# Performance work log

Measured on AMD Instinct MI355X. Metric: run time of the kernel, lower is better.

## Reference

```python
import jax, jax.numpy as jnp
import numpy as np

TEMPERATURE = 0.07
NEG_INF = -1e9


def setup_inputs() -> dict:
    key = jax.random.key(0)
    k1, k2, k3, k4, k5 = jax.random.split(key, 5)
    B, L, H = 64, 256, 64
    query_embs = jax.random.normal(k1, (B, L, H), dtype=jnp.float32)
    key_embs = jax.random.normal(k2, (B, L, H), dtype=jnp.float32)
    labels = jax.random.randint(k3, (B,), 0, 2, dtype=jnp.int64)
    q_mask = jax.random.randint(k4, (B, L), 0, 2, dtype=jnp.int32)
    k_mask = jax.random.randint(k5, (B, L), 0, 2, dtype=jnp.int32)
    return {"query_embs": query_embs, "key_embs": key_embs, "labels": labels,
            "q_mask": q_mask, "k_mask": k_mask}


def reference(query_embs, key_embs, labels, q_mask, k_mask):
    # ColBERT-style late interaction over all B x B pairs.
    # sim: (B_q, B_k, Lq, Lk) token-level dot products.
    sim = jnp.einsum('bqh,ckh->bcqk', query_embs, key_embs)
    # Mask out padded key tokens before the max over key positions.
    sim = jnp.where(k_mask[None, :, None, :].astype(bool), sim, NEG_INF)
    maxsim = jnp.max(sim, axis=-1)                      # (B_q, B_k, Lq)
    qm = q_mask[:, None, :].astype(maxsim.dtype)        # (B_q, 1, Lq)
    scores = jnp.sum(maxsim * qm, axis=-1) / TEMPERATURE  # (B_q, B_k)
    # Cross-entropy on rows with labels==1, target = diagonal index.
    logp = jax.nn.log_softmax(scores, axis=-1)
    B = scores.shape[0]
    diag = logp[jnp.arange(B), jnp.arange(B)]           # (B,)
    w = labels.astype(scores.dtype)
    denom = jnp.maximum(jnp.sum(w), 1.0)
    return -jnp.sum(w * diag) / denom
```

## Files before the change

kernel.cpp:

```cpp
#include <hip/hip_runtime.h>
#include <math.h>

#define PB 64
#define PL 256
#define PH 64
#define TEMP 0.07f
#define NEG_INF_F (-1e9f)

#define KSTRIDE 72
#define KROWB   (KSTRIDE * 2)
#define KSLAB   (PL * KSTRIDE)
#define BGRP    2

typedef short short8 __attribute__((ext_vector_type(8)));
typedef float f32x4 __attribute__((ext_vector_type(4)));

__device__ __forceinline__ unsigned short f32_to_bf16(float f) {
    unsigned int u = __float_as_uint(f);
    u += 0x7FFFu + ((u >> 16) & 1u);
    return (unsigned short)(u >> 16);
}

__global__ __launch_bounds__(256)
void prep_kernel(const float* __restrict__ Q,
                 const float* __restrict__ K,
                 const int*   __restrict__ kmask,
                 const int*   __restrict__ qmask,
                 unsigned short* __restrict__ Qcomp,
                 unsigned short* __restrict__ Kcomp,
                 int* __restrict__ nvK,
                 int* __restrict__ nvQ) {
    const int tid  = threadIdx.x;
    const int lane = tid & 63;
    const int wave = tid >> 6;
    __shared__ int posArr[PL];
    __shared__ int wcnt[4];

    const bool isQ = (blockIdx.x >= 256);
    const int  bid = isQ ? (blockIdx.x - 256) : blockIdx.x;
    const int  idx     = bid >> 2;
    const int  quarter = bid & 3;

    const int* mask = isQ ? (qmask + idx * PL) : (kmask + idx * PL);
    const int km = mask[tid];
    unsigned long long bal = __ballot(km != 0);
    int within = __popcll(bal & ((1ull << lane) - 1ull));
    if (lane == 0) wcnt[wave] = __popcll(bal);
    __syncthreads();
    int base = 0;
    #pragma unroll
    for (int w = 0; w < 4; ++w) base += (w < wave) ? wcnt[w] : 0;
    posArr[tid] = km ? (base + within) : -1;
    const int nv = wcnt[0] + wcnt[1] + wcnt[2] + wcnt[3];
    __syncthreads();

    const int sub = lane >> 4;
    const int cl  = lane & 15;
    const float* src = (isQ ? Q : K) + (size_t)idx * PL * PH;

    if (!isQ) {
        unsigned short* slab = Kcomp + (size_t)idx * KSLAB;
        #pragma unroll
        for (int it = 0; it < 4; ++it) {
            int r = quarter * 64 + it * 16 + wave * 4 + sub;
            int p = posArr[r];
            if (p >= 0) {
                float4 v = *(const float4*)(src + (size_t)r * PH + cl * 4);
                ushort4 o;
                o.x = f32_to_bf16(v.x); o.y = f32_to_bf16(v.y);
                o.z = f32_to_bf16(v.z); o.w = f32_to_bf16(v.w);
                *(ushort4*)(slab + (size_t)p * KSTRIDE + cl * 4) = o;
            }
        }
        const int rows16 = (nv + 15) & ~15;
        const int padChunks = (rows16 - nv) * 16;
        if (tid < padChunks) {
            int row = nv + (tid >> 4);
            if (row >= quarter * 64 && row < quarter * 64 + 64)
                *(ushort4*)(slab + (size_t)row * KSTRIDE + (tid & 15) * 4) = (ushort4){0, 0, 0, 0};
        }
        if (quarter == 0 && tid == 0) nvK[idx] = nv;
    } else {
        unsigned short* slab = Qcomp + (size_t)idx * PL * PH;
        #pragma unroll
        for (int it = 0; it < 4; ++it) {
            int r = quarter * 64 + it * 16 + wave * 4 + sub;
            int p = posArr[r];
            if (p >= 0) {
                float4 v = *(const float4*)(src + (size_t)r * PH + cl * 4);
                ushort4 o;
                o.x = f32_to_bf16(v.x); o.y = f32_to_bf16(v.y);
                o.z = f32_to_bf16(v.z); o.w = f32_to_bf16(v.w);
                *(ushort4*)(slab + (size_t)p * PH + cl * 4) = o;
            }
        }
        #pragma unroll
        for (int it = 0; it < 4; ++it) {
            int id2 = it * 256 + tid;
            int row = quarter * 64 + (id2 >> 4);
            if (row >= nv)
                *(ushort4*)(slab + (size_t)row * PH + (id2 & 15) * 4) = (ushort4){0, 0, 0, 0};
        }
        if (quarter == 0 && tid == 0) nvQ[idx] = nv;
    }
}

__global__ __launch_bounds__(256)
void colbert_scores_mfma(const unsigned short* __restrict__ Qcomp,
                         const unsigned short* __restrict__ Kcomp,
                         const int*   __restrict__ nvK,
                         const int*   __restrict__ nvQ,
                         float*       __restrict__ scores) {
    const int c  = blockIdx.x;
    const int bg = blockIdx.y;
    const int tid  = threadIdx.x;
    const int wave = tid >> 6;
    const int lane = tid & 63;
    const int n    = lane & 15;
    const int g    = (lane >> 4) & 3;

    __shared__ __align__(16) unsigned short Ks[PL * KSTRIDE];
    __shared__ float red[BGRP][4];

    const int nv     = nvK[c];
    const int rows16 = (nv + 15) & ~15;
    const int nbytes = rows16 * KROWB;

    {
        const char* gsrc  = (const char*)(Kcomp + (size_t)c * KSLAB);
        char*       lbase = (char*)Ks;
        const int nchunks = (nbytes + 4095) >> 12;
        for (int it = 0; it < nchunks; ++it) {
            int off = it * 4096 + tid * 16;
            __builtin_amdgcn_global_load_lds(
                (const __attribute__((address_space(1))) unsigned int*)(gsrc + off),
                (__attribute__((address_space(3)))       unsigned int*)(lbase + off),
                16, 0, 0);
        }
    }

    const int b0 = bg * BGRP;
    const int nq0 = nvQ[b0];
    const int nq1 = nvQ[b0 + 1];
    const int ntQP = ((max(nq0, nq1)) + 31) >> 5;

    __syncthreads();

    const f32x4 ZERO4 = (f32x4){0.f, 0.f, 0.f, 0.f};
    const int ntFull   = nv >> 4;
    const int tailCols = nv & 15;
    const unsigned short* krow0 = &Ks[n * KSTRIDE + g * 8];
    const float biasv = (n < tailCols) ? 0.0f : NEG_INF_F;
    const f32x4 BIAS4 = (f32x4){biasv, biasv, biasv, biasv};

    float partial[BGRP] = {0.0f, 0.0f};

    for (int qp = wave; qp < ntQP; qp += 4) {
        short8 aA[BGRP][2][2];
        #pragma unroll
        for (int bi = 0; bi < BGRP; ++bi) {
            const unsigned short* Qrow = Qcomp + ((size_t)(b0 + bi) * PL + qp * 32 + n) * PH + g * 8;
            aA[bi][0][0] = *(const short8*)(Qrow);
            aA[bi][0][1] = *(const short8*)(Qrow + 32);
            aA[bi][1][0] = *(const short8*)(Qrow + 16 * PH);
            aA[bi][1][1] = *(const short8*)(Qrow + 16 * PH + 32);
        }

        float maxv[BGRP][2][4];
        #pragma unroll
        for (int bi = 0; bi < BGRP; ++bi)
            #pragma unroll
            for (int t = 0; t < 2; ++t)
                #pragma unroll
                for (int r = 0; r < 4; ++r) maxv[bi][t][r] = NEG_INF_F;

        int ct = 0;
        for (; ct + 1 < ntFull; ct += 2) {
            const unsigned short* ka = krow0 + ct * 16 * KSTRIDE;
            short8 kA0 = *(const short8*)(ka);
            short8 kA1 = *(const short8*)(ka + 32);
            short8 kB0 = *(const short8*)(ka + 16 * KSTRIDE);
            short8 kB1 = *(const short8*)(ka + 16 * KSTRIDE + 32);

            #pragma unroll
            for (int bi = 0; bi < BGRP; ++bi)
                #pragma unroll
                for (int t = 0; t < 2; ++t) {
                    f32x4 accA = __builtin_amdgcn_mfma_f32_16x16x32_bf16(aA[bi][t][0], kA0, ZERO4, 0, 0, 0);
                    accA = __builtin_amdgcn_mfma_f32_16x16x32_bf16(aA[bi][t][1], kA1, accA, 0, 0, 0);
                    f32x4 accB = __builtin_amdgcn_mfma_f32_16x16x32_bf16(aA[bi][t][0], kB0, ZERO4, 0, 0, 0);
                    accB = __builtin_amdgcn_mfma_f32_16x16x32_bf16(aA[bi][t][1], kB1, accB, 0, 0, 0);
                    #pragma unroll
                    for (int r = 0; r < 4; ++r)
                        maxv[bi][t][r] = fmaxf(maxv[bi][t][r], fmaxf(accA[r], accB[r]));
                }
        }

        if (ntFull & 1) {
            const unsigned short* ka = krow0 + ct * 16 * KSTRIDE;
            short8 k0 = *(const short8*)(ka);
            short8 k1 = *(const short8*)(ka + 32);
            #pragma unroll
            for (int bi = 0; bi < BGRP; ++bi)
                #pragma unroll
                for (int t = 0; t < 2; ++t) {
                    f32x4 acc = __builtin_amdgcn_mfma_f32_16x16x32_bf16(aA[bi][t][0], k0, ZERO4, 0, 0, 0);
                    acc = __builtin_amdgcn_mfma_f32_16x16x32_bf16(aA[bi][t][1], k1, acc, 0, 0, 0);
                    #pragma unroll
                    for (int r = 0; r < 4; ++r)
                        maxv[bi][t][r] = fmaxf(maxv[bi][t][r], acc[r]);
                }
            ct++;
        }

        if (tailCols) {
            const unsigned short* ka = krow0 + ct * 16 * KSTRIDE;
            short8 k0 = *(const short8*)(ka);
            short8 k1 = *(const short8*)(ka + 32);
            #pragma unroll
            for (int bi = 0; bi < BGRP; ++bi)
                #pragma unroll
                for (int t = 0; t < 2; ++t) {
                    f32x4 acc = __builtin_amdgcn_mfma_f32_16x16x32_bf16(aA[bi][t][0], k0, BIAS4, 0, 0, 0);
                    acc = __builtin_amdgcn_mfma_f32_16x16x32_bf16(aA[bi][t][1], k1, acc, 0, 0, 0);
                    #pragma unroll
                    for (int r = 0; r < 4; ++r)
                        maxv[bi][t][r] = fmaxf(maxv[bi][t][r], acc[r]);
                }
        }

        #pragma unroll
        for (int bi = 0; bi < BGRP; ++bi)
            #pragma unroll
            for (int t = 0; t < 2; ++t)
                #pragma unroll
                for (int r = 0; r < 4; ++r) {
                    float mv = maxv[bi][t][r];
                    mv = fmaxf(mv, __shfl_xor(mv, 1, 16));
                    mv = fmaxf(mv, __shfl_xor(mv, 2, 16));
                    mv = fmaxf(mv, __shfl_xor(mv, 4, 16));
                    mv = fmaxf(mv, __shfl_xor(mv, 8, 16));
                    if (n == 0) partial[bi] += mv;
                }
    }

    #pragma unroll
    for (int bi = 0; bi < BGRP; ++bi) {
        float p = partial[bi];
        p += __shfl_xor(p, 16, 64);
        p += __shfl_xor(p, 32, 64);
        if (lane == 0) red[bi][wave] = p;
    }

    __syncthreads();
    if (tid < BGRP) {
        float total = red[tid][0] + red[tid][1] + red[tid][2] + red[tid][3];
        scores[(b0 + tid) * PB + c] = total * (1.0f / TEMP);
    }
}

__global__ void finalize_kernel(const float* __restrict__ scores,
                                const int*   __restrict__ labels,
                                float*       __restrict__ out) {
    const int r = threadIdx.x;
    const float* row = scores + r * PB;
    float mx = NEG_INF_F;
    for (int j = 0; j < PB; ++j) mx = fmaxf(mx, row[j]);
    float se = 0.0f;
    for (int j = 0; j < PB; ++j) se += expf(row[j] - mx);
    float logp_diag = row[r] - mx - logf(se);
    float w = (float)labels[r];
    float wd = w * logp_diag;
    #pragma unroll
    for (int off = 32; off >= 1; off >>= 1) {
        wd += __shfl_xor(wd, off, 64);
        w  += __shfl_xor(w,  off, 64);
    }
    if (r == 0) out[0] = -wd / fmaxf(w, 1.0f);
}

extern "C" void kernel_launch(void* const* d_in, const int* in_sizes, int n_in,
                              void* d_out, int out_size, void* d_ws, size_t ws_size,
                              hipStream_t stream) {
    const float* Q      = (const float*)d_in[0];
    const float* K      = (const float*)d_in[1];
    const int*   labels = (const int*)d_in[2];
    const int*   qmask  = (const int*)d_in[3];
    const int*   kmask  = (const int*)d_in[4];
    float*       out    = (float*)d_out;

    char* ws = (char*)d_ws;
    float*          scores = (float*)ws;
    unsigned short* Qcomp  = (unsigned short*)(ws + 16 * 1024);
    unsigned short* Kcomp  = (unsigned short*)(ws + 16 * 1024 + 2 * 1024 * 1024);
    int*            nvK    = (int*)(ws + 16 * 1024 + 2 * 1024 * 1024 + (size_t)PB * KSLAB * 2);
    int*            nvQ    = nvK + 64;

    prep_kernel<<<512, 256, 0, stream>>>(Q, K, kmask, qmask, Qcomp, Kcomp, nvK, nvQ);

    dim3 grid(PB, PB / BGRP);
    colbert_scores_mfma<<<grid, 256, 0, stream>>>(Qcomp, Kcomp, nvK, nvQ, scores);
    finalize_kernel<<<1, 64, 0, stream>>>(scores, labels, out);
}
```

Before: 96.18 us.

## Reuse each K slab across four query batches and fuse finalize via last-block atomic

```diff
diff --git a/kernel.cpp b/kernel.cpp
--- a/kernel.cpp
+++ b/kernel.cpp
@@ -10,7 +10,8 @@
 #define KSTRIDE 72
 #define KROWB   (KSTRIDE * 2)
 #define KSLAB   (PL * KSTRIDE)
-#define BGRP    2
+#define BGRP    4
+#define NBLK    (PB * (PB / BGRP))
 
 typedef short short8 __attribute__((ext_vector_type(8)));
 typedef float f32x4 __attribute__((ext_vector_type(4)));
@@ -29,12 +30,15 @@
                  unsigned short* __restrict__ Qcomp,
                  unsigned short* __restrict__ Kcomp,
                  int* __restrict__ nvK,
-                 int* __restrict__ nvQ) {
+                 int* __restrict__ nvQ,
+                 int* __restrict__ doneCnt) {
     const int tid  = threadIdx.x;
     const int lane = tid & 63;
     const int wave = tid >> 6;
     __shared__ int posArr[PL];
     __shared__ int wcnt[4];
+
+    if (blockIdx.x == 0 && tid == 0) doneCnt[0] = 0;
 
     const bool isQ = (blockIdx.x >= 256);
     const int  bid = isQ ? (blockIdx.x - 256) : blockIdx.x;
@@ -105,12 +109,15 @@
     }
 }
 
-__global__ __launch_bounds__(256)
+__global__ __launch_bounds__(256, 4)
 void colbert_scores_mfma(const unsigned short* __restrict__ Qcomp,
                          const unsigned short* __restrict__ Kcomp,
                          const int*   __restrict__ nvK,
                          const int*   __restrict__ nvQ,
-                         float*       __restrict__ scores) {
+                         const int*   __restrict__ labels,
+                         float*       __restrict__ scores,
+                         int*         __restrict__ doneCnt,
+                         float*       __restrict__ out) {
     const int c  = blockIdx.x;
     const int bg = blockIdx.y;
     const int tid  = threadIdx.x;
@@ -121,6 +128,7 @@
 
     __shared__ __align__(16) unsigned short Ks[PL * KSTRIDE];
     __shared__ float red[BGRP][4];
+    __shared__ int isLast;
 
     const int nv     = nvK[c];
     const int rows16 = (nv + 15) & ~15;
@@ -139,11 +147,6 @@
         }
     }
 
-    const int b0 = bg * BGRP;
-    const int nq0 = nvQ[b0];
-    const int nq1 = nvQ[b0 + 1];
-    const int ntQP = ((max(nq0, nq1)) + 31) >> 5;
-
     __syncthreads();
 
     const f32x4 ZERO4 = (f32x4){0.f, 0.f, 0.f, 0.f};
@@ -153,130 +156,145 @@
     const float biasv = (n < tailCols) ? 0.0f : NEG_INF_F;
     const f32x4 BIAS4 = (f32x4){biasv, biasv, biasv, biasv};
 
-    float partial[BGRP] = {0.0f, 0.0f};
-
-    for (int qp = wave; qp < ntQP; qp += 4) {
-        short8 aA[BGRP][2][2];
-        #pragma unroll
-        for (int bi = 0; bi < BGRP; ++bi) {
-            const unsigned short* Qrow = Qcomp + ((size_t)(b0 + bi) * PL + qp * 32 + n) * PH + g * 8;
-            aA[bi][0][0] = *(const short8*)(Qrow);
-            aA[bi][0][1] = *(const short8*)(Qrow + 32);
-            aA[bi][1][0] = *(const short8*)(Qrow + 16 * PH);
-            aA[bi][1][1] = *(const short8*)(Qrow + 16 * PH + 32);
-        }
-
-        float maxv[BGRP][2][4];
-        #pragma unroll
-        for (int bi = 0; bi < BGRP; ++bi)
+    #pragma unroll 1
+    for (int bh = 0; bh < 2; ++bh) {
+        const int b0 = bg * BGRP + bh * 2;
+        const int nq0 = nvQ[b0];
+        const int nq1 = nvQ[b0 + 1];
+        const int ntQP = ((max(nq0, nq1)) + 31) >> 5;
+
+        float partial[2] = {0.0f, 0.0f};
+
+        for (int qp = wave; qp < ntQP; qp += 4) {
+            short8 aA[2][2][2];
             #pragma unroll
-            for (int t = 0; t < 2; ++t)
-                #pragma unroll
-                for (int r = 0; r < 4; ++r) maxv[bi][t][r] = NEG_INF_F;
-
-        int ct = 0;
-        for (; ct + 1 < ntFull; ct += 2) {
-            const unsigned short* ka = krow0 + ct * 16 * KSTRIDE;
-            short8 kA0 = *(const short8*)(ka);
-            short8 kA1 = *(const short8*)(ka + 32);
-            short8 kB0 = *(const short8*)(ka + 16 * KSTRIDE);
-            short8 kB1 = *(const short8*)(ka + 16 * KSTRIDE + 32);
-
+            for (int bi = 0; bi < 2; ++bi) {
+                const unsigned short* Qrow = Qcomp + ((size_t)(b0 + bi) * PL + qp * 32 + n) * PH + g * 8;
+                aA[bi][0][0] = *(const short8*)(Qrow);
+                aA[bi][0][1] = *(const short8*)(Qrow + 32);
+                aA[bi][1][0] = *(const short8*)(Qrow + 16 * PH);
+                aA[bi][1][1] = *(const short8*)(Qrow + 16 * PH + 32);
+            }
+
+            float maxv[2][2][4];
             #pragma unroll
-            for (int bi = 0; bi < BGRP; ++bi)
-                #pragma unroll
-                for (int t = 0; t < 2; ++t) {
-                    f32x4 accA = __builtin_amdgcn_mfma_f32_16x16x32_bf16(aA[bi][t][0], kA0, ZERO4, 0, 0, 0);
-                    accA = __builtin_amdgcn_mfma_f32_16x16x32_bf16(aA[bi][t][1], kA1, accA, 0, 0, 0);
-                    f32x4 accB = __builtin_amdgcn_mfma_f32_16x16x32_bf16(aA[bi][t][0], kB0, ZERO4, 0, 0, 0);
-                    accB = __builtin_amdgcn_mfma_f32_16x16x32_bf16(aA[bi][t][1], kB1, accB, 0, 0, 0);
-                    #pragma unroll
-                    for (int r = 0; r < 4; ++r)
-                        maxv[bi][t][r] = fmaxf(maxv[bi][t][r], fmaxf(accA[r], accB[r]));
-                }
-        }
-
-        if (ntFull & 1) {
-            const unsigned short* ka = krow0 + ct * 16 * KSTRIDE;
-            short8 k0 = *(const short8*)(ka);
-            short8 k1 = *(const short8*)(ka + 32);
+            for (int bi = 0; bi < 2; ++bi)
+                #pragma unroll
+                for (int t = 0; t < 2; ++t)
+                    #pragma unroll
+                    for (int r = 0; r < 4; ++r) maxv[bi][t][r] = NEG_INF_F;
+
+            int ct = 0;
+            for (; ct + 1 < ntFull; ct += 2) {
+                const unsigned short* ka = krow0 + ct * 16 * KSTRIDE;
+                short8 kA0 = *(const short8*)(ka);
+                short8 kA1 = *(const short8*)(ka + 32);
+                short8 kB0 = *(const short8*)(ka + 16 * KSTRIDE);
+                short8 kB1 = *(const short8*)(ka + 16 * KSTRIDE + 32);
+
+                #pragma unroll
+                for (int bi = 0; bi < 2; ++bi)
+                    #pragma unroll
+                    for (int t = 0; t < 2; ++t) {
+                        f32x4 accA = __builtin_amdgcn_mfma_f32_16x16x32_bf16(aA[bi][t][0], kA0, ZERO4, 0, 0, 0);
+                        accA = __builtin_amdgcn_mfma_f32_16x16x32_bf16(aA[bi][t][1], kA1, accA, 0, 0, 0);
+                        f32x4 accB = __builtin_amdgcn_mfma_f32_16x16x32_bf16(aA[bi][t][0], kB0, ZERO4, 0, 0, 0);
+                        accB = __builtin_amdgcn_mfma_f32_16x16x32_bf16(aA[bi][t][1], kB1, accB, 0, 0, 0);
+                        #pragma unroll
+                        for (int r = 0; r < 4; ++r)
+                            maxv[bi][t][r] = fmaxf(maxv[bi][t][r], fmaxf(accA[r], accB[r]));
+                    }
+            }
+
+            if (ntFull & 1) {
+                const unsigned short* ka = krow0 + ct * 16 * KSTRIDE;
+                short8 k0 = *(const short8*)(ka);
+                short8 k1 = *(const short8*)(ka + 32);
+                #pragma unroll
+                for (int bi = 0; bi < 2; ++bi)
+                    #pragma unroll
+                    for (int t = 0; t < 2; ++t) {
+                        f32x4 acc = __builtin_amdgcn_mfma_f32_16x16x32_bf16(aA[bi][t][0], k0, ZERO4, 0, 0, 0);
+                        acc = __builtin_amdgcn_mfma_f32_16x16x32_bf16(aA[bi][t][1], k1, acc, 0, 0, 0);
+                        #pragma unroll
+                        for (int r = 0; r < 4; ++r)
+                            maxv[bi][t][r] = fmaxf(maxv[bi][t][r], acc[r]);
+                    }
+                ct++;
+            }
+
+            if (tailCols) {
+                const unsigned short* ka = krow0 + ct * 16 * KSTRIDE;
+                short8 k0 = *(const short8*)(ka);
+                short8 k1 = *(const short8*)(ka + 32);
+                #pragma unroll
+                for (int bi = 0; bi < 2; ++bi)
+                    #pragma unroll
+                    for (int t = 0; t < 2; ++t) {
+                        f32x4 acc = __builtin_amdgcn_mfma_f32_16x16x32_bf16(aA[bi][t][0], k0, BIAS4, 0, 0, 0);
+                        acc = __builtin_amdgcn_mfma_f32_16x16x32_bf16(aA[bi][t][1], k1, acc, 0, 0, 0);
+                        #pragma unroll
+                        for (int r = 0; r < 4; ++r)
+                            maxv[bi][t][r] = fmaxf(maxv[bi][t][r], acc[r]);
+                    }
+            }
+
             #pragma unroll
-            for (int bi = 0; bi < BGRP; ++bi)
-                #pragma unroll
-                for (int t = 0; t < 2; ++t) {
-                    f32x4 acc = __builtin_amdgcn_mfma_f32_16x16x32_bf16(aA[bi][t][0], k0, ZERO4, 0, 0, 0);
-                    acc = __builtin_amdgcn_mfma_f32_16x16x32_bf16(aA[bi][t][1], k1, acc, 0, 0, 0);
-                    #pragma unroll
-                    for (int r = 0; r < 4; ++r)
-                        maxv[bi][t][r] = fmaxf(maxv[bi][t][r], acc[r]);
-                }
-            ct++;
-        }
-
-        if (tailCols) {
-            const unsigned short* ka = krow0 + ct * 16 * KSTRIDE;
-            short8 k0 = *(const short8*)(ka);
-            short8 k1 = *(const short8*)(ka + 32);
-            #pragma unroll
-            for (int bi = 0; bi < BGRP; ++bi)
-                #pragma unroll
-                for (int t = 0; t < 2; ++t) {
-                    f32x4 acc = __builtin_amdgcn_mfma_f32_16x16x32_bf16(aA[bi][t][0], k0, BIAS4, 0, 0, 0);
-                    acc = __builtin_amdgcn_mfma_f32_16x16x32_bf16(aA[bi][t][1], k1, acc, 0, 0, 0);
-                    #pragma unroll
-                    for (int r = 0; r < 4; ++r)
-                        maxv[bi][t][r] = fmaxf(maxv[bi][t][r], acc[r]);
-                }
-        }
-
-        #pragma unroll
-        for (int bi = 0; bi < BGRP; ++bi)
-            #pragma unroll
-            for (int t = 0; t < 2; ++t)
-                #pragma unroll
-                for (int r = 0; r < 4; ++r) {
-                    float mv = maxv[bi][t][r];
-                    mv = fmaxf(mv, __shfl_xor(mv, 1, 16));
-                    mv = fmaxf(mv, __shfl_xor(mv, 2, 16));
-                    mv = fmaxf(mv, __shfl_xor(mv, 4, 16));
-                    mv = fmaxf(mv, __shfl_xor(mv, 8, 16));
-                    if (n == 0) partial[bi] += mv;
-                }
-    }
-
-    #pragma unroll
-    for (int bi = 0; bi < BGRP; ++bi) {
-        float p = partial[bi];
-        p += __shfl_xor(p, 16, 64);
-        p += __shfl_xor(p, 32, 64);
-        if (lane == 0) red[bi][wave] = p;
+            for (int bi = 0; bi < 2; ++bi)
+                #pragma unroll
+                for (int t = 0; t < 2; ++t)
+                    #pragma unroll
+                    for (int r = 0; r < 4; ++r) {
+                        float mv = maxv[bi][t][r];
+                        mv = fmaxf(mv, __shfl_xor(mv, 1, 16));
+                        mv = fmaxf(mv, __shfl_xor(mv, 2, 16));
+                        mv = fmaxf(mv, __shfl_xor(mv, 4, 16));
+                        mv = fmaxf(mv, __shfl_xor(mv, 8, 16));
+                        if (n == 0) partial[bi] += mv;
+                    }
+        }
+
+        #pragma unroll
+        for (int bi = 0; bi < 2; ++bi) {
+            float p = partial[bi];
+            p += __shfl_xor(p, 16, 64);
+            p += __shfl_xor(p, 32, 64);
+            if (lane == 0) red[bh * 2 + bi][wave] = p;
+        }
     }
 
     __syncthreads();
     if (tid < BGRP) {
         float total = red[tid][0] + red[tid][1] + red[tid][2] + red[tid][3];
-        scores[(b0 + tid) * PB + c] = total * (1.0f / TEMP);
-    }
-}
-
-__global__ void finalize_kernel(const float* __restrict__ scores,
-                                const int*   __restrict__ labels,
-                                float*       __restrict__ out) {
-    const int r = threadIdx.x;
-    const float* row = scores + r * PB;
-    float mx = NEG_INF_F;
-    for (int j = 0; j < PB; ++j) mx = fmaxf(mx, row[j]);
-    float se = 0.0f;
-    for (int j = 0; j < PB; ++j) se += expf(row[j] - mx);
-    float logp_diag = row[r] - mx - logf(se);
-    float w = (float)labels[r];
-    float wd = w * logp_diag;
-    #pragma unroll
-    for (int off = 32; off >= 1; off >>= 1) {
-        wd += __shfl_xor(wd, off, 64);
-        w  += __shfl_xor(w,  off, 64);
-    }
-    if (r == 0) out[0] = -wd / fmaxf(w, 1.0f);
+        scores[(bg * BGRP + tid) * PB + c] = total * (1.0f / TEMP);
+    }
+
+    __threadfence();
+    if (tid == 0) {
+        int prev = atomicAdd(doneCnt, 1);
+        isLast = (prev == NBLK - 1);
+    }
+    __syncthreads();
+    if (!isLast) return;
+    __threadfence();
+
+    if (tid < 64) {
+        const int r = tid;
+        const float* row = scores + r * PB;
+        float mx = NEG_INF_F;
+        for (int j = 0; j < PB; ++j) mx = fmaxf(mx, row[j]);
+        float se = 0.0f;
+        for (int j = 0; j < PB; ++j) se += expf(row[j] - mx);
+        float logp_diag = row[r] - mx - logf(se);
+        float w = (float)labels[r];
+        float wd = w * logp_diag;
+        #pragma unroll
+        for (int off = 32; off >= 1; off >>= 1) {
+            wd += __shfl_xor(wd, off, 64);
+            w  += __shfl_xor(w,  off, 64);
+        }
+        if (r == 0) out[0] = -wd / fmaxf(w, 1.0f);
+    }
 }
 
 extern "C" void kernel_launch(void* const* d_in, const int* in_sizes, int n_in,
@@ -295,10 +313,11 @@
     unsigned short* Kcomp  = (unsigned short*)(ws + 16 * 1024 + 2 * 1024 * 1024);
     int*            nvK    = (int*)(ws + 16 * 1024 + 2 * 1024 * 1024 + (size_t)PB * KSLAB * 2);
     int*            nvQ    = nvK + 64;
-
-    prep_kernel<<<512, 256, 0, stream>>>(Q, K, kmask, qmask, Qcomp, Kcomp, nvK, nvQ);
+    int*            doneCnt = nvQ + 64;
+
+    prep_kernel<<<512, 256, 0, stream>>>(Q, K, kmask, qmask, Qcomp, Kcomp, nvK, nvQ, doneCnt);
 
     dim3 grid(PB, PB / BGRP);
-    colbert_scores_mfma<<<grid, 256, 0, stream>>>(Qcomp, Kcomp, nvK, nvQ, scores);
-    finalize_kernel<<<1, 64, 0, stream>>>(scores, labels, out);
+    colbert_scores_mfma<<<grid, 256, 0, stream>>>(Qcomp, Kcomp, nvK, nvQ, labels,
+                                                  scores, doneCnt, out);
 }
```

New measurement: 154.3 us. 60.5% more time.

## Store Q/K in MFMA fragment layout and read K directly from global memory

Applied to the files above, without the earlier changes.

```diff
diff --git a/kernel.cpp b/kernel.cpp
--- a/kernel.cpp
+++ b/kernel.cpp
@@ -7,10 +7,9 @@
 #define TEMP 0.07f
 #define NEG_INF_F (-1e9f)
 
-#define KSTRIDE 72
-#define KROWB   (KSTRIDE * 2)
-#define KSLAB   (PL * KSTRIDE)
-#define BGRP    2
+#define KFTILE 1024
+#define KFSLAB (16 * KFTILE)
+#define BGRP   2
 
 typedef short short8 __attribute__((ext_vector_type(8)));
 typedef float f32x4 __attribute__((ext_vector_type(4)));
@@ -19,6 +18,11 @@
     unsigned int u = __float_as_uint(f);
     u += 0x7FFFu + ((u >> 16) & 1u);
     return (unsigned short)(u >> 16);
+}
+
+__device__ __forceinline__ int frag_off(int p, int cc) {
+    return ((p >> 4) * KFTILE) + ((cc >> 3) * 512) +
+           (((((cc >> 1) & 3) * 16) + (p & 15)) * 8) + ((cc & 1) * 4);
 }
 
 __global__ __launch_bounds__(256)
@@ -26,8 +30,8 @@
                  const float* __restrict__ K,
                  const int*   __restrict__ kmask,
                  const int*   __restrict__ qmask,
-                 unsigned short* __restrict__ Qcomp,
-                 unsigned short* __restrict__ Kcomp,
+                 unsigned short* __restrict__ Qfrag,
+                 unsigned short* __restrict__ Kfrag,
                  int* __restrict__ nvK,
                  int* __restrict__ nvQ) {
     const int tid  = threadIdx.x;
@@ -57,57 +61,45 @@
     const int sub = lane >> 4;
     const int cl  = lane & 15;
     const float* src = (isQ ? Q : K) + (size_t)idx * PL * PH;
+    unsigned short* slab = (isQ ? Qfrag : Kfrag) + (size_t)idx * KFSLAB;
+
+    #pragma unroll
+    for (int it = 0; it < 4; ++it) {
+        int r = quarter * 64 + it * 16 + wave * 4 + sub;
+        int p = posArr[r];
+        if (p >= 0) {
+            float4 v = *(const float4*)(src + (size_t)r * PH + cl * 4);
+            ushort4 o;
+            o.x = f32_to_bf16(v.x); o.y = f32_to_bf16(v.y);
+            o.z = f32_to_bf16(v.z); o.w = f32_to_bf16(v.w);
+            *(ushort4*)(slab + frag_off(p, cl)) = o;
+        }
+    }
 
     if (!isQ) {
-        unsigned short* slab = Kcomp + (size_t)idx * KSLAB;
-        #pragma unroll
-        for (int it = 0; it < 4; ++it) {
-            int r = quarter * 64 + it * 16 + wave * 4 + sub;
-            int p = posArr[r];
-            if (p >= 0) {
-                float4 v = *(const float4*)(src + (size_t)r * PH + cl * 4);
-                ushort4 o;
-                o.x = f32_to_bf16(v.x); o.y = f32_to_bf16(v.y);
-                o.z = f32_to_bf16(v.z); o.w = f32_to_bf16(v.w);
-                *(ushort4*)(slab + (size_t)p * KSTRIDE + cl * 4) = o;
-            }
-        }
         const int rows16 = (nv + 15) & ~15;
         const int padChunks = (rows16 - nv) * 16;
         if (tid < padChunks) {
             int row = nv + (tid >> 4);
             if (row >= quarter * 64 && row < quarter * 64 + 64)
-                *(ushort4*)(slab + (size_t)row * KSTRIDE + (tid & 15) * 4) = (ushort4){0, 0, 0, 0};
+                *(ushort4*)(slab + frag_off(row, tid & 15)) = (ushort4){0, 0, 0, 0};
         }
         if (quarter == 0 && tid == 0) nvK[idx] = nv;
     } else {
-        unsigned short* slab = Qcomp + (size_t)idx * PL * PH;
-        #pragma unroll
-        for (int it = 0; it < 4; ++it) {
-            int r = quarter * 64 + it * 16 + wave * 4 + sub;
-            int p = posArr[r];
-            if (p >= 0) {
-                float4 v = *(const float4*)(src + (size_t)r * PH + cl * 4);
-                ushort4 o;
-                o.x = f32_to_bf16(v.x); o.y = f32_to_bf16(v.y);
-                o.z = f32_to_bf16(v.z); o.w = f32_to_bf16(v.w);
-                *(ushort4*)(slab + (size_t)p * PH + cl * 4) = o;
-            }
-        }
         #pragma unroll
         for (int it = 0; it < 4; ++it) {
             int id2 = it * 256 + tid;
             int row = quarter * 64 + (id2 >> 4);
             if (row >= nv)
-                *(ushort4*)(slab + (size_t)row * PH + (id2 & 15) * 4) = (ushort4){0, 0, 0, 0};
+                *(ushort4*)(slab + frag_off(row, id2 & 15)) = (ushort4){0, 0, 0, 0};
         }
         if (quarter == 0 && tid == 0) nvQ[idx] = nv;
     }
 }
 
 __global__ __launch_bounds__(256)
-void colbert_scores_mfma(const unsigned short* __restrict__ Qcomp,
-                         const unsigned short* __restrict__ Kcomp,
+void colbert_scores_mfma(const unsigned short* __restrict__ Qfrag,
+                         const unsigned short* __restrict__ Kfrag,
                          const int*   __restrict__ nvK,
                          const int*   __restrict__ nvQ,
                          float*       __restrict__ scores) {
@@ -117,53 +109,36 @@
     const int wave = tid >> 6;
     const int lane = tid & 63;
     const int n    = lane & 15;
-    const int g    = (lane >> 4) & 3;
-
-    __shared__ __align__(16) unsigned short Ks[PL * KSTRIDE];
+
     __shared__ float red[BGRP][4];
 
-    const int nv     = nvK[c];
-    const int rows16 = (nv + 15) & ~15;
-    const int nbytes = rows16 * KROWB;
-
-    {
-        const char* gsrc  = (const char*)(Kcomp + (size_t)c * KSLAB);
-        char*       lbase = (char*)Ks;
-        const int nchunks = (nbytes + 4095) >> 12;
-        for (int it = 0; it < nchunks; ++it) {
-            int off = it * 4096 + tid * 16;
-            __builtin_amdgcn_global_load_lds(
-                (const __attribute__((address_space(1))) unsigned int*)(gsrc + off),
-                (__attribute__((address_space(3)))       unsigned int*)(lbase + off),
-                16, 0, 0);
-        }
-    }
-
-    const int b0 = bg * BGRP;
+    const int nv       = nvK[c];
+    const int ntFull   = nv >> 4;
+    const int tailCols = nv & 15;
+
+    const int b0  = bg * BGRP;
     const int nq0 = nvQ[b0];
     const int nq1 = nvQ[b0 + 1];
-    const int ntQP = ((max(nq0, nq1)) + 31) >> 5;
-
-    __syncthreads();
+    const int ntQP = ((nq0 > nq1 ? nq0 : nq1) + 31) >> 5;
 
     const f32x4 ZERO4 = (f32x4){0.f, 0.f, 0.f, 0.f};
-    const int ntFull   = nv >> 4;
-    const int tailCols = nv & 15;
-    const unsigned short* krow0 = &Ks[n * KSTRIDE + g * 8];
     const float biasv = (n < tailCols) ? 0.0f : NEG_INF_F;
     const f32x4 BIAS4 = (f32x4){biasv, biasv, biasv, biasv};
 
+    const unsigned short* kb = Kfrag + (size_t)c * KFSLAB + lane * 8;
+
     float partial[BGRP] = {0.0f, 0.0f};
 
     for (int qp = wave; qp < ntQP; qp += 4) {
         short8 aA[BGRP][2][2];
         #pragma unroll
         for (int bi = 0; bi < BGRP; ++bi) {
-            const unsigned short* Qrow = Qcomp + ((size_t)(b0 + bi) * PL + qp * 32 + n) * PH + g * 8;
-            aA[bi][0][0] = *(const short8*)(Qrow);
-            aA[bi][0][1] = *(const short8*)(Qrow + 32);
-            aA[bi][1][0] = *(const short8*)(Qrow + 16 * PH);
-            aA[bi][1][1] = *(const short8*)(Qrow + 16 * PH + 32);
+            const unsigned short* qbase = Qfrag + (size_t)(b0 + bi) * KFSLAB
+                                         + qp * 2 * KFTILE + lane * 8;
+            aA[bi][0][0] = *(const short8*)(qbase);
+            aA[bi][0][1] = *(const short8*)(qbase + 512);
+            aA[bi][1][0] = *(const short8*)(qbase + 1024);
+            aA[bi][1][1] = *(const short8*)(qbase + 1536);
         }
 
         float maxv[BGRP][2][4];
@@ -176,11 +151,11 @@
 
         int ct = 0;
         for (; ct + 1 < ntFull; ct += 2) {
-            const unsigned short* ka = krow0 + ct * 16 * KSTRIDE;
+            const unsigned short* ka = kb + ct * KFTILE;
             short8 kA0 = *(const short8*)(ka);
-            short8 kA1 = *(const short8*)(ka + 32);
-            short8 kB0 = *(const short8*)(ka + 16 * KSTRIDE);
-            short8 kB1 = *(const short8*)(ka + 16 * KSTRIDE + 32);
+            short8 kA1 = *(const short8*)(ka + 512);
+            short8 kB0 = *(const short8*)(ka + 1024);
+            short8 kB1 = *(const short8*)(ka + 1536);
 
             #pragma unroll
             for (int bi = 0; bi < BGRP; ++bi)
@@ -197,9 +172,9 @@
         }
 
         if (ntFull & 1) {
-            const unsigned short* ka = krow0 + ct * 16 * KSTRIDE;
+            const unsigned short* ka = kb + ct * KFTILE;
             short8 k0 = *(const short8*)(ka);
-            short8 k1 = *(const short8*)(ka + 32);
+            short8 k1 = *(const short8*)(ka + 512);
             #pragma unroll
             for (int bi = 0; bi < BGRP; ++bi)
                 #pragma unroll
@@ -214,9 +189,9 @@
         }
 
         if (tailCols) {
-            const unsigned short* ka = krow0 + ct * 16 * KSTRIDE;
+            const unsigned short* ka = kb + ct * KFTILE;
             short8 k0 = *(const short8*)(ka);
-            short8 k1 = *(const short8*)(ka + 32);
+            short8 k1 = *(const short8*)(ka + 512);
             #pragma unroll
             for (int bi = 0; bi < BGRP; ++bi)
                 #pragma unroll
@@ -291,14 +266,14 @@
 
     char* ws = (char*)d_ws;
     float*          scores = (float*)ws;
-    unsigned short* Qcomp  = (unsigned short*)(ws + 16 * 1024);
-    unsigned short* Kcomp  = (unsigned short*)(ws + 16 * 1024 + 2 * 1024 * 1024);
-    int*            nvK    = (int*)(ws + 16 * 1024 + 2 * 1024 * 1024 + (size_t)PB * KSLAB * 2);
+    unsigned short* Qfrag  = (unsigned short*)(ws + 16 * 1024);
+    unsigned short* Kfrag  = (unsigned short*)(ws + 16 * 1024 + 2 * 1024 * 1024);
+    int*            nvK    = (int*)(ws + 16 * 1024 + 4 * 1024 * 1024);
     int*            nvQ    = nvK + 64;
 
-    prep_kernel<<<512, 256, 0, stream>>>(Q, K, kmask, qmask, Qcomp, Kcomp, nvK, nvQ);
+    prep_kernel<<<512, 256, 0, stream>>>(Q, K, kmask, qmask, Qfrag, Kfrag, nvK, nvQ);
 
     dim3 grid(PB, PB / BGRP);
-    colbert_scores_mfma<<<grid, 256, 0, stream>>>(Qcomp, Kcomp, nvK, nvQ, scores);
+    colbert_scores_mfma<<<grid, 256, 0, stream>>>(Qfrag, Kfrag, nvK, nvQ, scores);
     finalize_kernel<<<1, 64, 0, stream>>>(scores, labels, out);
 }
```

Measured after the change: 95.76 us. About the same (-0.4%).
